# Performance work log

Measured on AMD Instinct MI355X. Metric: run time of the kernel, lower is better.

Reference implementation:

```python
import jax, jax.numpy as jnp
import numpy as np

NUM_USERS = 100000
NUM_ITEMS = 200000
IN_DIM = 128
HID = 256
E = 500000


def setup_inputs() -> dict:
    key = jax.random.key(0)
    ks = jax.random.split(key, 12)
    s1 = 1.0 / np.sqrt(2 * IN_DIM)
    s2 = 1.0 / np.sqrt(HID)
    return {
        "user_embed": jax.random.normal(ks[0], (NUM_USERS, IN_DIM), jnp.float32),
        "item_embed": jax.random.normal(ks[1], (NUM_ITEMS, IN_DIM), jnp.float32),
        "u_clicks": jax.random.randint(ks[2], (E,), 0, NUM_USERS, jnp.int32),
        "v_clicks": jax.random.randint(ks[3], (E,), 0, NUM_ITEMS, jnp.int32),
        "u_buys": jax.random.randint(ks[4], (E,), 0, NUM_USERS, jnp.int32),
        "v_buys": jax.random.randint(ks[5], (E,), 0, NUM_ITEMS, jnp.int32),
        "W1_clicks": jax.random.normal(ks[6], (2 * IN_DIM, HID), jnp.float32) * s1,
        "b1_clicks": jnp.zeros((HID,), jnp.float32),
        "W2_clicks": jax.random.normal(ks[7], (HID,), jnp.float32) * s2,
        "b2_clicks": jnp.zeros((1,), jnp.float32),
        "W1_buys": jax.random.normal(ks[8], (2 * IN_DIM, HID), jnp.float32) * s1,
        "b1_buys": jnp.zeros((HID,), jnp.float32),
        "W2_buys": jax.random.normal(ks[9], (HID,), jnp.float32) * s2,
        "b2_buys": jnp.zeros((1,), jnp.float32),
    }


def _edge_mlp(h_u, h_v, W1, b1, W2, b2):
    # concat([h_u, h_v]) @ W1 computed without materializing the concat:
    # split W1 into source-half and target-half. Dropout(p=0) is identity.
    d = h_u.shape[1]
    h = jax.nn.relu(h_u @ W1[:d] + h_v @ W1[d:] + b1)  # [E, HID]
    return h @ W2 + b2[0]  # [E] (Linear(hidden,1).squeeze(1))


def reference(user_embed, item_embed, u_clicks, v_clicks, u_buys, v_buys,
              W1_clicks, b1_clicks, W2_clicks, b2_clicks,
              W1_buys, b1_buys, W2_buys, b2_buys):
    logits_clicks = _edge_mlp(user_embed[u_clicks], item_embed[v_clicks],
                              W1_clicks, b1_clicks, W2_clicks, b2_clicks)
    logits_buys = _edge_mlp(user_embed[u_buys], item_embed[v_buys],
                            W1_buys, b1_buys, W2_buys, b2_buys)
    return logits_clicks, logits_buys
```

## Files before the change

### kernel.cpp

```cpp
#include <hip/hip_runtime.h>
#include <hip/hip_bf16.h>

typedef short bf16x8 __attribute__((ext_vector_type(8)));
typedef float f32x4 __attribute__((ext_vector_type(4)));

#define HID 256
#define IN_DIM 128
#define M_BLOCK 64
#define LDS_STRIDE 264

__device__ __forceinline__ float bf2f(unsigned short x) {
    union { unsigned int u; float f; } c; c.u = ((unsigned int)x) << 16; return c.f;
}
__device__ __forceinline__ unsigned short f2bf(float f) {
    union { float f; unsigned int u; } c; c.f = f;
    unsigned int u = c.u;
    u += 0x7FFFu + ((u >> 16) & 1u);
    return (unsigned short)(u >> 16);
}
__device__ __forceinline__ unsigned int pack2(float lo, float hi) {
    return (unsigned int)f2bf(lo) | ((unsigned int)f2bf(hi) << 16);
}

__device__ __forceinline__ bool detect_bf16(const unsigned short* p, int strideElems) {
    const int lane = threadIdx.x & 63;
    unsigned int u = p[(size_t)2 * lane * strideElems];
    unsigned int e = (u >> 7) & 0xFFu;
    bool bad = ((u & 0x7FFFu) != 0u) && (e < 90u || e > 141u);
    return __ballot(bad) == 0ull;
}
__device__ __forceinline__ bool detect_idx64(const int* p) {
    const int lane = threadIdx.x & 63;
    int v = p[2 * (lane * 64) + 1];
    return __ballot(v != 0) == 0ull;
}

extern "C" __global__ void pack_w1_kernel(
    const void* __restrict__ W1c,
    const void* __restrict__ W1b,
    unsigned short* __restrict__ outp)
{
    const int t = blockIdx.y;
    const void* W1 = t ? W1b : W1c;
    const unsigned short* W1u = (const unsigned short*)W1;
    const float* W1f = (const float*)W1;
    const bool w1bf = detect_bf16(W1u, 512);

    const int tid = blockIdx.x * 256 + threadIdx.x;
    const int lane = tid & 63;
    const int nt = (tid >> 6) & 15;
    const int kt = tid >> 10;
    const int k0 = kt * 32 + (lane >> 4) * 8;
    const int n  = nt * 16 + (lane & 15);
    unsigned short vals[8];
#pragma unroll
    for (int j = 0; j < 8; ++j) {
        const int src = (k0 + j) * HID + n;
        vals[j] = w1bf ? W1u[src] : f2bf(W1f[src]);
    }
    unsigned short* dst = outp + (size_t)t * 65536 + (size_t)tid * 8;
    *reinterpret_cast<uint4*>(dst) = *reinterpret_cast<const uint4*>(vals);
}

extern "C" __global__ __launch_bounds__(256, 3)
void edge_mlp_kernel(
    const void* __restrict__ user_embed,
    const void* __restrict__ item_embed,
    const int* __restrict__ u0, const int* __restrict__ v0,
    const int* __restrict__ u1, const int* __restrict__ v1,
    const unsigned short* __restrict__ packedW1,
    const void* __restrict__ b1_0, const void* __restrict__ w2_0,
    const void* __restrict__ b2_0,
    const void* __restrict__ b1_1, const void* __restrict__ w2_1,
    const void* __restrict__ b2_1,
    float* __restrict__ out, int E)
{
    __shared__ unsigned short sA[M_BLOCK * LDS_STRIDE];
    __shared__ float pRed[4][M_BLOCK];

    const int t  = blockIdx.y;
    const int e0 = blockIdx.x * M_BLOCK;
    const int tid = threadIdx.x;

    const int* uI = t ? u1 : u0;
    const int* vI = t ? v1 : v0;
    const void* b1 = t ? b1_1 : b1_0;
    const void* w2 = t ? w2_1 : w2_0;
    const void* b2 = t ? b2_1 : b2_0;
    const unsigned short* pW = packedW1 + (size_t)t * 65536;

    const bool uBf  = detect_bf16((const unsigned short*)user_embed, 1024);
    const bool iBf  = detect_bf16((const unsigned short*)item_embed, 1024);
    const bool w2Bf = detect_bf16((const unsigned short*)w2, 2);
    const bool u64f = detect_idx64(uI);
    const bool v64f = detect_idx64(vI);

    {
        const int el = tid >> 2;
        const int q  = tid & 3;
        const int e  = e0 + el;
        uint4* dst = reinterpret_cast<uint4*>(&sA[el * LDS_STRIDE + q * 64]);
        if (e < E) {
            size_t idx; const void* tab; bool tbf; int off;
            if (q < 2) { idx = (size_t)(u64f ? uI[2 * e] : uI[e]); tab = user_embed; tbf = uBf; off = q * 64; }
            else       { idx = (size_t)(v64f ? vI[2 * e] : vI[e]); tab = item_embed; tbf = iBf; off = (q - 2) * 64; }
            if (tbf) {
                const uint4* s4 = reinterpret_cast<const uint4*>(
                    (const unsigned short*)tab + idx * IN_DIM + off);
#pragma unroll
                for (int i = 0; i < 8; ++i) dst[i] = s4[i];
            } else {
                const float4* s4 = reinterpret_cast<const float4*>(
                    (const float*)tab + idx * IN_DIM + off);
#pragma unroll
                for (int i = 0; i < 8; ++i) {
                    float4 f0 = s4[2 * i];
                    float4 f1 = s4[2 * i + 1];
                    uint4 o;
                    o.x = pack2(f0.x, f0.y);
                    o.y = pack2(f0.z, f0.w);
                    o.z = pack2(f1.x, f1.y);
                    o.w = pack2(f1.z, f1.w);
                    dst[i] = o;
                }
            }
        } else {
            uint4 z; z.x = z.y = z.z = z.w = 0;
#pragma unroll
            for (int i = 0; i < 8; ++i) dst[i] = z;
        }
    }
    __syncthreads();

    const int wv   = tid >> 6;
    const int lane = tid & 63;
    const int lq   = lane >> 4;
    const int lm   = lane & 15;

    f32x4 acc[4][4];
#pragma unroll
    for (int ms = 0; ms < 4; ++ms)
#pragma unroll
        for (int ntg = 0; ntg < 4; ++ntg)
            acc[ms][ntg] = (f32x4){0.f, 0.f, 0.f, 0.f};

#pragma unroll
    for (int kt = 0; kt < 8; ++kt) {
        const int koff = kt * 32 + lq * 8;
        bf16x8 aF[4];
#pragma unroll
        for (int ms = 0; ms < 4; ++ms)
            aF[ms] = *reinterpret_cast<const bf16x8*>(&sA[(ms * 16 + lm) * LDS_STRIDE + koff]);
#pragma unroll
        for (int ntg = 0; ntg < 4; ++ntg) {
            const int nt = wv * 4 + ntg;
            bf16x8 bF = *reinterpret_cast<const bf16x8*>(
                pW + (((size_t)(kt * 16 + nt) * 64 + lane) * 8));
#pragma unroll
            for (int ms = 0; ms < 4; ++ms)
                acc[ms][ntg] = __builtin_amdgcn_mfma_f32_16x16x32_bf16(aF[ms], bF, acc[ms][ntg], 0, 0, 0);
        }
    }

    float part[4][4];
#pragma unroll
    for (int ms = 0; ms < 4; ++ms)
#pragma unroll
        for (int r = 0; r < 4; ++r) part[ms][r] = 0.f;

#pragma unroll
    for (int ntg = 0; ntg < 4; ++ntg) {
        const int n = (wv * 4 + ntg) * 16 + lm;
        const float b1n = w2Bf ? bf2f(((const unsigned short*)b1)[n]) : ((const float*)b1)[n];
        const float w2n = w2Bf ? bf2f(((const unsigned short*)w2)[n]) : ((const float*)w2)[n];
#pragma unroll
        for (int ms = 0; ms < 4; ++ms)
#pragma unroll
            for (int r = 0; r < 4; ++r) {
                float h = acc[ms][ntg][r] + b1n;
                h = fmaxf(h, 0.f);
                part[ms][r] = fmaf(h, w2n, part[ms][r]);
            }
    }

#pragma unroll
    for (int off = 1; off < 16; off <<= 1) {
#pragma unroll
        for (int ms = 0; ms < 4; ++ms)
#pragma unroll
            for (int r = 0; r < 4; ++r)
                part[ms][r] += __shfl_xor(part[ms][r], off, 64);
    }

    if (lm == 0) {
#pragma unroll
        for (int ms = 0; ms < 4; ++ms)
#pragma unroll
            for (int r = 0; r < 4; ++r)
                pRed[wv][ms * 16 + lq * 4 + r] = part[ms][r];
    }
    __syncthreads();

    if (tid < M_BLOCK) {
        const int e = e0 + tid;
        if (e < E) {
            const float b2v = w2Bf ? bf2f(((const unsigned short*)b2)[0]) : ((const float*)b2)[0];
            float s = b2v + pRed[0][tid] + pRed[1][tid] + pRed[2][tid] + pRed[3][tid];
            out[(size_t)t * E + e] = s;
        }
    }
}

extern "C" void kernel_launch(void* const* d_in, const int* in_sizes, int n_in,
                              void* d_out, int out_size, void* d_ws, size_t ws_size,
                              hipStream_t stream)
{
    const void* user_embed = d_in[0];
    const void* item_embed = d_in[1];
    const int* u0 = (const int*)d_in[2];
    const int* v0 = (const int*)d_in[3];
    const int* u1 = (const int*)d_in[4];
    const int* v1 = (const int*)d_in[5];
    const void* W1c = d_in[6];
    const void* b1c = d_in[7];
    const void* w2c = d_in[8];
    const void* b2c = d_in[9];
    const void* W1b = d_in[10];
    const void* b1b = d_in[11];
    const void* w2b = d_in[12];
    const void* b2b = d_in[13];

    const int E = in_sizes[2];
    unsigned short* packedW1 = (unsigned short*)d_ws;

    hipLaunchKernelGGL(pack_w1_kernel, dim3(32, 2), dim3(256), 0, stream, W1c, W1b, packedW1);

    dim3 grid((E + M_BLOCK - 1) / M_BLOCK, 2);
    hipLaunchKernelGGL(edge_mlp_kernel, grid, dim3(256), 0, stream,
                       user_embed, item_embed, u0, v0, u1, v1, packedW1,
                       b1c, w2c, b2c, b1b, w2b, b2b,
                       (float*)d_out, E);
}
```

Baseline: 469.7 us.

## Pre-convert embedding tables to bf16 and gather rows directly into LDS

Adds a pass that converts the full user and item tables to bf16 in workspace, so the per-edge gather reads half the bytes from a compact table that better fits in cache. The gather now uses global-to-LDS direct loads into an MFMA-friendly per-wave layout instead of register staging with a padded row stride. Occupancy target is raised to four blocks. The trade-off is a full-table conversion on every call and a dependence on a large workspace; the old conversion path is kept as a fallback when it is not available.

New measurement: 424.8 us. 9.6% less time.

```diff
diff --git a/kernel.cpp b/kernel.cpp
--- a/kernel.cpp
+++ b/kernel.cpp
@@ -7,7 +7,6 @@
 #define HID 256
 #define IN_DIM 128
 #define M_BLOCK 64
-#define LDS_STRIDE 264
 
 __device__ __forceinline__ float bf2f(unsigned short x) {
     union { unsigned int u; float f; } c; c.u = ((unsigned int)x) << 16; return c.f;
@@ -20,6 +19,13 @@
 }
 __device__ __forceinline__ unsigned int pack2(float lo, float hi) {
     return (unsigned int)f2bf(lo) | ((unsigned int)f2bf(hi) << 16);
+}
+
+__device__ __forceinline__ void gload_lds16(const void* g, void* l) {
+    __builtin_amdgcn_global_load_lds(
+        (const __attribute__((address_space(1))) void*)g,
+        (__attribute__((address_space(3))) void*)l,
+        16, 0, 0);
 }
 
 __device__ __forceinline__ bool detect_bf16(const unsigned short* p, int strideElems) {
@@ -33,6 +39,37 @@
     const int lane = threadIdx.x & 63;
     int v = p[2 * (lane * 64) + 1];
     return __ballot(v != 0) == 0ull;
+}
+
+extern "C" __global__ void cvt_tables_kernel(
+    const void* __restrict__ user_embed, const void* __restrict__ item_embed,
+    unsigned short* __restrict__ uT, unsigned short* __restrict__ iT,
+    long long nU8, long long nI8)
+{
+    const int t = blockIdx.y;
+    const void* src = t ? item_embed : user_embed;
+    unsigned short* dst = t ? iT : uT;
+    const long long n8 = t ? nI8 : nU8;
+    const bool bf = detect_bf16((const unsigned short*)src, 1024);
+    long long i = (long long)blockIdx.x * 256 + threadIdx.x;
+    const long long stride = (long long)gridDim.x * 256;
+    if (bf) {
+        const uint4* s = (const uint4*)src;
+        for (; i < n8; i += stride)
+            *reinterpret_cast<uint4*>(dst + i * 8) = s[i];
+    } else {
+        const float4* s = (const float4*)src;
+        for (; i < n8; i += stride) {
+            float4 f0 = s[2 * i];
+            float4 f1 = s[2 * i + 1];
+            uint4 o;
+            o.x = pack2(f0.x, f0.y);
+            o.y = pack2(f0.z, f0.w);
+            o.z = pack2(f1.x, f1.y);
+            o.w = pack2(f1.z, f1.w);
+            *reinterpret_cast<uint4*>(dst + i * 8) = o;
+        }
+    }
 }
 
 extern "C" __global__ void pack_w1_kernel(
@@ -62,10 +99,12 @@
     *reinterpret_cast<uint4*>(dst) = *reinterpret_cast<const uint4*>(vals);
 }
 
-extern "C" __global__ __launch_bounds__(256, 3)
+extern "C" __global__ __launch_bounds__(256, 4)
 void edge_mlp_kernel(
     const void* __restrict__ user_embed,
     const void* __restrict__ item_embed,
+    const unsigned short* __restrict__ uT,
+    const unsigned short* __restrict__ iT,
     const int* __restrict__ u0, const int* __restrict__ v0,
     const int* __restrict__ u1, const int* __restrict__ v1,
     const unsigned short* __restrict__ packedW1,
@@ -73,14 +112,16 @@
     const void* __restrict__ b2_0,
     const void* __restrict__ b1_1, const void* __restrict__ w2_1,
     const void* __restrict__ b2_1,
-    float* __restrict__ out, int E)
-{
-    __shared__ unsigned short sA[M_BLOCK * LDS_STRIDE];
+    float* __restrict__ out, int E, int useWs)
+{
+    __shared__ __attribute__((aligned(16))) unsigned short sA[32 * 64 * 8];
     __shared__ float pRed[4][M_BLOCK];
 
     const int t  = blockIdx.y;
     const int e0 = blockIdx.x * M_BLOCK;
     const int tid = threadIdx.x;
+    const int lane = tid & 63;
+    const int wv = tid >> 6;
 
     const int* uI = t ? u1 : u0;
     const int* vI = t ? v1 : v0;
@@ -89,53 +130,53 @@
     const void* b2 = t ? b2_1 : b2_0;
     const unsigned short* pW = packedW1 + (size_t)t * 65536;
 
-    const bool uBf  = detect_bf16((const unsigned short*)user_embed, 1024);
-    const bool iBf  = detect_bf16((const unsigned short*)item_embed, 1024);
     const bool w2Bf = detect_bf16((const unsigned short*)w2, 2);
-    const bool u64f = detect_idx64(uI);
-    const bool v64f = detect_idx64(vI);
 
     {
-        const int el = tid >> 2;
-        const int q  = tid & 3;
-        const int e  = e0 + el;
-        uint4* dst = reinterpret_cast<uint4*>(&sA[el * LDS_STRIDE + q * 64]);
-        if (e < E) {
-            size_t idx; const void* tab; bool tbf; int off;
-            if (q < 2) { idx = (size_t)(u64f ? uI[2 * e] : uI[e]); tab = user_embed; tbf = uBf; off = q * 64; }
-            else       { idx = (size_t)(v64f ? vI[2 * e] : vI[e]); tab = item_embed; tbf = iBf; off = (q - 2) * 64; }
+        const int* gI = (wv < 2) ? uI : vI;
+        const bool g64 = detect_idx64(gI);
+        const int e = e0 + lane;
+        const int eC = (e < E) ? e : (E - 1);
+        const size_t idx = (size_t)(g64 ? gI[2 * eC] : gI[eC]);
+
+        if (useWs) {
+            const unsigned short* tab = (wv < 2) ? uT : iT;
+            const unsigned short* rowbase = tab + idx * IN_DIM + (wv & 1) * 64;
+            unsigned short* sbase = &sA[(wv * 8) * 512];
+#pragma unroll
+            for (int c = 0; c < 8; ++c)
+                gload_lds16(rowbase + c * 8, sbase + c * 512);
+        } else {
+            const void* tab = (wv < 2) ? user_embed : item_embed;
+            const bool tbf = detect_bf16((const unsigned short*)tab, 1024);
             if (tbf) {
-                const uint4* s4 = reinterpret_cast<const uint4*>(
-                    (const unsigned short*)tab + idx * IN_DIM + off);
-#pragma unroll
-                for (int i = 0; i < 8; ++i) dst[i] = s4[i];
+                const unsigned short* rowbase =
+                    (const unsigned short*)tab + idx * IN_DIM + (wv & 1) * 64;
+                unsigned short* sbase = &sA[(wv * 8) * 512];
+#pragma unroll
+                for (int c = 0; c < 8; ++c)
+                    gload_lds16(rowbase + c * 8, sbase + c * 512);
             } else {
-                const float4* s4 = reinterpret_cast<const float4*>(
-                    (const float*)tab + idx * IN_DIM + off);
-#pragma unroll
-                for (int i = 0; i < 8; ++i) {
-                    float4 f0 = s4[2 * i];
-                    float4 f1 = s4[2 * i + 1];
+                const float* rowbase =
+                    (const float*)tab + idx * IN_DIM + (wv & 1) * 64;
+#pragma unroll
+                for (int c = 0; c < 8; ++c) {
+                    float4 f0 = *reinterpret_cast<const float4*>(rowbase + c * 8);
+                    float4 f1 = *reinterpret_cast<const float4*>(rowbase + c * 8 + 4);
                     uint4 o;
                     o.x = pack2(f0.x, f0.y);
                     o.y = pack2(f0.z, f0.w);
                     o.z = pack2(f1.x, f1.y);
                     o.w = pack2(f1.z, f1.w);
-                    dst[i] = o;
+                    *reinterpret_cast<uint4*>(&sA[((wv * 8 + c) * 64 + lane) * 8]) = o;
                 }
             }
-        } else {
-            uint4 z; z.x = z.y = z.z = z.w = 0;
-#pragma unroll
-            for (int i = 0; i < 8; ++i) dst[i] = z;
         }
     }
     __syncthreads();
 
-    const int wv   = tid >> 6;
-    const int lane = tid & 63;
-    const int lq   = lane >> 4;
-    const int lm   = lane & 15;
+    const int lq = lane >> 4;
+    const int lm = lane & 15;
 
     f32x4 acc[4][4];
 #pragma unroll
@@ -146,11 +187,11 @@
 
 #pragma unroll
     for (int kt = 0; kt < 8; ++kt) {
-        const int koff = kt * 32 + lq * 8;
         bf16x8 aF[4];
 #pragma unroll
         for (int ms = 0; ms < 4; ++ms)
-            aF[ms] = *reinterpret_cast<const bf16x8*>(&sA[(ms * 16 + lm) * LDS_STRIDE + koff]);
+            aF[ms] = *reinterpret_cast<const bf16x8*>(
+                &sA[(((kt * 4 + lq) * 64) + ms * 16 + lm) * 8]);
 #pragma unroll
         for (int ntg = 0; ntg < 4; ++ntg) {
             const int nt = wv * 4 + ntg;
@@ -158,7 +199,8 @@
                 pW + (((size_t)(kt * 16 + nt) * 64 + lane) * 8));
 #pragma unroll
             for (int ms = 0; ms < 4; ++ms)
-                acc[ms][ntg] = __builtin_amdgcn_mfma_f32_16x16x32_bf16(aF[ms], bF, acc[ms][ntg], 0, 0, 0);
+                acc[ms][ntg] = __builtin_amdgcn_mfma_f32_16x16x32_bf16(
+                    aF[ms], bF, acc[ms][ntg], 0, 0, 0);
         }
     }
 
@@ -231,13 +273,27 @@
     const void* b2b = d_in[13];
 
     const int E = in_sizes[2];
+    const size_t U = (size_t)in_sizes[0] / IN_DIM;
+    const size_t I = (size_t)in_sizes[1] / IN_DIM;
+
     unsigned short* packedW1 = (unsigned short*)d_ws;
+    unsigned short* uT = (unsigned short*)((char*)d_ws + 262144);
+    unsigned short* iT = uT + U * IN_DIM;
+    const size_t need = 262144 + (U + I) * IN_DIM * sizeof(unsigned short);
+    const int useWs = (ws_size >= need) ? 1 : 0;
+
+    if (useWs) {
+        const long long nU8 = (long long)U * IN_DIM / 8;
+        const long long nI8 = (long long)I * IN_DIM / 8;
+        hipLaunchKernelGGL(cvt_tables_kernel, dim3(4096, 2), dim3(256), 0, stream,
+                           user_embed, item_embed, uT, iT, nU8, nI8);
+    }
 
     hipLaunchKernelGGL(pack_w1_kernel, dim3(32, 2), dim3(256), 0, stream, W1c, W1b, packedW1);
 
     dim3 grid((E + M_BLOCK - 1) / M_BLOCK, 2);
     hipLaunchKernelGGL(edge_mlp_kernel, grid, dim3(256), 0, stream,
-                       user_embed, item_embed, u0, v0, u1, v1, packedW1,
+                       user_embed, item_embed, uT, iT, u0, v0, u1, v1, packedW1,
                        b1c, w2c, b2c, b1b, w2b, b2b,
-                       (float*)d_out, E);
-}
+                       (float*)d_out, E, useWs);
+}
```
